# Kernel tuning notes

Hardware: AMD Instinct MI355X
Metric: run time of the kernel (lower is better)

The kernel has to match this reference:

```python
import jax, jax.numpy as jnp
import numpy as np

NUM_HEADS = 8


def setup_inputs() -> dict:
    key = jax.random.key(0)
    ks = jax.random.split(key, 5)
    b, c, h, w = 8, 256, 32, 32
    x = jax.random.normal(ks[0], (b, c, h, w), dtype=jnp.float32)
    w_qkv = jax.random.normal(ks[1], (3 * c, c), dtype=jnp.float32) * (c ** -0.5)
    b_qkv = jax.random.normal(ks[2], (3 * c,), dtype=jnp.float32) * 0.02
    w_proj = jax.random.normal(ks[3], (c, c), dtype=jnp.float32) * (c ** -0.5)
    b_proj = jax.random.normal(ks[4], (c,), dtype=jnp.float32) * 0.02
    return {"x": x, "w_qkv": w_qkv, "b_qkv": b_qkv, "w_proj": w_proj, "b_proj": b_proj}


def reference(x, w_qkv, b_qkv, w_proj, b_proj):
    b, c, h, w = x.shape
    nh = NUM_HEADS
    dh = c // nh
    L = h * w
    scale = dh ** -0.5
    # 1x1 conv == per-pixel GEMM
    qkv = jnp.einsum('bchw,oc->bohw', x, w_qkv) + b_qkv[None, :, None, None]
    qkv = qkv.reshape(b, 3, nh, dh, L)
    q, k, v = qkv[:, 0], qkv[:, 1], qkv[:, 2]  # each (b, nh, dh, L)
    attn = jnp.einsum('bhdi,bhdj->bhij', q, k) * scale  # (b, nh, L, L)
    attn = jax.nn.softmax(attn, axis=-1)
    out = jnp.einsum('bhdj,bhij->bhdi', v, attn)  # (b, nh, dh, L)
    out = out.reshape(b, c, h, w)
    proj = jnp.einsum('bchw,oc->bohw', out, w_proj) + b_proj[None, :, None, None]
    return x + proj
```

## Files before the change

kernel.cpp:

```cpp
#include <hip/hip_runtime.h>
#include <math.h>

#define B_   8
#define CIN  256
#define L_   1024
#define NH_  8
#define DH_  32

typedef __attribute__((ext_vector_type(8))) short short8;
typedef __attribute__((ext_vector_type(4))) short short4v;
typedef __attribute__((ext_vector_type(4))) float f32x4;
typedef __attribute__((ext_vector_type(16))) float f32x16;
typedef __attribute__((ext_vector_type(4))) unsigned int uint4v;

__device__ inline short f2bf_hu(float f) {
    union { float f; unsigned u; } v; v.f = f;
    return (short)((v.u + 0x8000u) >> 16);
}
__device__ inline float bf2f(short s) {
    union { unsigned u; float f; } v; v.u = ((unsigned)(unsigned short)s) << 16;
    return v.f;
}
__device__ inline unsigned pkbf2(float a, float b) {
    union { float f; unsigned u; } x, y; x.f = a; y.f = b;
    return __builtin_amdgcn_perm(y.u + 0x8000u, x.u + 0x8000u, 0x07060302u);
}

__global__ __launch_bounds__(256) void qkv_gemm(
    const float* __restrict__ x, const float* __restrict__ wq,
    const float* __restrict__ bias, short* __restrict__ qkv3)
{
    __shared__ __align__(16) short Xs[2][64][40];
    __shared__ __align__(16) short Wt[2][128][32];
    const int t = threadIdx.x, lane = t & 63, wv = t >> 6;
    const int n = lane & 15, quad = lane >> 4;
    const int b = blockIdx.z, o0 = blockIdx.y * 128, l0 = blockIdx.x * 64;

    float bias_r[8];
    #pragma unroll
    for (int nf = 0; nf < 8; nf++) bias_r[nf] = bias[o0 + nf * 16 + n];

    f32x4 acc[8];
    #pragma unroll
    for (int nf = 0; nf < 8; nf++) acc[nf] = (f32x4){0.f, 0.f, 0.f, 0.f};

    const int cS = t >> 3, lsS = (t & 7) * 8;

    const int ow = t >> 1, hw = t & 1;
    const float* wp = wq + (size_t)(o0 + ow) * 256 + hw * 16;
    const int wssw = (ow >> 1) & 3;
    float4 wr0, wr1, wr2, wr3;
    auto loadW = [&]() {
        wr0 = ((const float4*)wp)[0]; wr1 = ((const float4*)wp)[1];
        wr2 = ((const float4*)wp)[2]; wr3 = ((const float4*)wp)[3];
        wp += 32;
    };
    auto wwrite = [&](int buf) {
        uint4v pa = { pkbf2(wr0.x, wr0.y), pkbf2(wr0.z, wr0.w),
                      pkbf2(wr1.x, wr1.y), pkbf2(wr1.z, wr1.w) };
        uint4v pb = { pkbf2(wr2.x, wr2.y), pkbf2(wr2.z, wr2.w),
                      pkbf2(wr3.x, wr3.y), pkbf2(wr3.z, wr3.w) };
        *(uint4v*)&Wt[buf][ow][((hw * 2)     ^ wssw) * 8] = pa;
        *(uint4v*)&Wt[buf][ow][((hw * 2 + 1) ^ wssw) * 8] = pb;
    };

    auto xwrite = [&](int buf, const float4& a, const float4& c) {
        const float vals[8] = {a.x, a.y, a.z, a.w, c.x, c.y, c.z, c.w};
        #pragma unroll
        for (int k = 0; k < 8; k++) {
            const int ll = lsS + k;
            const int col = (((cS >> 3) ^ (ll & 3)) << 3) | (cS & 7);
            Xs[buf][ll][col] = f2bf_hu(vals[k]);
        }
    };

    const float* xp = &x[(((size_t)b * CIN + cS) << 10) + l0 + lsS];
    float4 xa = *(const float4*)xp, xb = *(const float4*)(xp + 4);
    loadW();
    xwrite(0, xa, xb);
    wwrite(0);
    xp += (size_t)32 << 10;
    xa = *(const float4*)xp; xb = *(const float4*)(xp + 4);
    loadW();

    const int wsw = (quad ^ ((n >> 1) & 3)) * 8;
    const int arow = wv * 16 + n;
    const int xsw = (quad ^ (arow & 3)) * 8;

    #pragma unroll
    for (int it = 0; it < 8; it++) {
        const int cur = it & 1;
        __syncthreads();
        const short8 af = *(const short8*)&Xs[cur][arow][xsw];
        #pragma unroll
        for (int nf = 0; nf < 8; nf++) {
            const short8 bf = *(const short8*)&Wt[cur][nf * 16 + n][wsw];
            acc[nf] = __builtin_amdgcn_mfma_f32_16x16x32_bf16(af, bf, acc[nf], 0, 0, 0);
        }
        if (it < 7) {
            xwrite(cur ^ 1, xa, xb);
            wwrite(cur ^ 1);
            if (it < 6) {
                xp += (size_t)32 << 10;
                xa = *(const float4*)xp; xb = *(const float4*)(xp + 4);
                loadW();
            }
        }
    }

    #pragma unroll
    for (int reg = 0; reg < 4; reg++) {
        const size_t l = l0 + wv * 16 + quad * 4 + reg;
        #pragma unroll
        for (int nf = 0; nf < 8; nf++) {
            const int o = o0 + nf * 16;
            const int tpl = o >> 8, hh = (o >> 5) & 7, dh0 = o & 31;
            short* dst = qkv3 + (((size_t)(tpl * 64 + b * 8 + hh)) << 15)
                              + l * 32 + dh0 + n;
            *dst = f2bf_hu(acc[nf][reg] + bias_r[nf]);
        }
    }
}

__global__ __launch_bounds__(256) void proj_gemm(
    const short* __restrict__ partO, const float* __restrict__ partD,
    const float* __restrict__ wq, const float* __restrict__ bias,
    const float* __restrict__ resid, float* __restrict__ out)
{
    __shared__ __align__(16) short Xs[2][64][40];
    __shared__ __align__(16) short Wt[2][64][32];
    const int t = threadIdx.x, lane = t & 63, wv = t >> 6;
    const int n = lane & 15, quad = lane >> 4;
    const int b = blockIdx.z, o0 = blockIdx.y * 64, l0 = blockIdx.x * 64;

    float bias_r[4];
    #pragma unroll
    for (int reg = 0; reg < 4; reg++) bias_r[reg] = bias[o0 + wv * 16 + quad * 4 + reg];

    f32x4 acc[4];
    #pragma unroll
    for (int nf = 0; nf < 4; nf++) acc[nf] = (f32x4){0.f, 0.f, 0.f, 0.f};

    const int l = t >> 2, cs = (t & 3) * 8;
    const size_t li = ((size_t)b << 10) + l0 + l;
    const short* p0 = &partO[(0 * (size_t)B_ * L_ + li) * CIN + cs];
    const short* p1 = &partO[(1 * (size_t)B_ * L_ + li) * CIN + cs];
    const float* pd0 = &partD[(0 * (size_t)B_ * L_ + li) * NH_];
    const float* pd1 = &partD[(1 * (size_t)B_ * L_ + li) * NH_];

    const int ow = t >> 2, cw = t & 3;
    const float* wp = wq + (size_t)(o0 + ow) * 256 + cw * 8;
    const int wpos = (cw ^ ((ow >> 1) & 3)) * 8;
    float4 wa, wb;
    auto loadW = [&]() {
        wa = ((const float4*)wp)[0]; wb = ((const float4*)wp)[1];
        wp += 32;
    };
    auto wwrite = [&](int buf) {
        uint4v pw = { pkbf2(wa.x, wa.y), pkbf2(wa.z, wa.w),
                      pkbf2(wb.x, wb.y), pkbf2(wb.z, wb.w) };
        *(uint4v*)&Wt[buf][ow][wpos] = pw;
    };

    short8 s0, s1;
    float d0, d1;
    auto combine_write = [&](int buf) {
        const float inv = 1.f / (d0 + d1);
        float v[8];
        #pragma unroll
        for (int e = 0; e < 8; e++) v[e] = (bf2f(s0[e]) + bf2f(s1[e])) * inv;
        uint4v pw = { pkbf2(v[0], v[1]), pkbf2(v[2], v[3]),
                      pkbf2(v[4], v[5]), pkbf2(v[6], v[7]) };
        *(uint4v*)&Xs[buf][l][cs] = pw;
    };

    s0 = *(const short8*)p0; s1 = *(const short8*)p1;
    d0 = pd0[0]; d1 = pd1[0];
    loadW();
    combine_write(0);
    wwrite(0);
    p0 += 32; p1 += 32;
    s0 = *(const short8*)p0; s1 = *(const short8*)p1;
    d0 = pd0[1]; d1 = pd1[1];
    loadW();

    const int wsw = (quad ^ ((n >> 1) & 3)) * 8;
    #pragma unroll
    for (int it = 0; it < 8; it++) {
        const int cur = it & 1;
        __syncthreads();
        const short8 af = *(const short8*)&Wt[cur][wv * 16 + n][wsw];
        #pragma unroll
        for (int nf = 0; nf < 4; nf++) {
            const short8 bf = *(const short8*)&Xs[cur][nf * 16 + n][quad * 8];
            acc[nf] = __builtin_amdgcn_mfma_f32_16x16x32_bf16(af, bf, acc[nf], 0, 0, 0);
        }
        if (it < 7) {
            combine_write(cur ^ 1);
            wwrite(cur ^ 1);
            if (it < 6) {
                p0 += 32; p1 += 32;
                s0 = *(const short8*)p0; s1 = *(const short8*)p1;
                d0 = pd0[it + 2]; d1 = pd1[it + 2];
                loadW();
            }
        }
    }

    #pragma unroll
    for (int reg = 0; reg < 4; reg++) {
        const int o = o0 + wv * 16 + quad * 4 + reg;
        #pragma unroll
        for (int nf = 0; nf < 4; nf++) {
            const size_t off = (((size_t)b * CIN + o) << 10) + l0 + nf * 16 + n;
            out[off] = acc[nf][reg] + bias_r[reg] + resid[off];
        }
    }
}

__global__ __launch_bounds__(256) void attn_mfma(
    const short* __restrict__ qkv3, short* __restrict__ partO,
    float* __restrict__ partD)
{
    __shared__ short Vt[2][32][80];

    const int t = threadIdx.x, lane = t & 63, wv = t >> 6;
    const int il = lane & 31, h2 = lane >> 5;
    const int id = blockIdx.x;
    const int bh = id & 63;
    const int b = bh >> 3, h = bh & 7;
    const int i0 = ((id >> 6) & 7) * 128;
    const int s  = id >> 9;

    const short* qbase = qkv3 + ((size_t)(b * 8 + h) << 15);
    const short* kbase = qbase + ((size_t)64 << 15);
    const short* vbase = qbase + ((size_t)128 << 15);

    const short* qp = qbase + (size_t)(i0 + wv * 32 + il) * 32 + h2 * 8;
    const short8 qa0 = *(const short8*)qp;
    const short8 qa1 = *(const short8*)(qp + 16);

    f32x16 o_acc = {0.f,0.f,0.f,0.f,0.f,0.f,0.f,0.f,
                    0.f,0.f,0.f,0.f,0.f,0.f,0.f,0.f};
    float dsum = 0.f;

    const float K1 = 0.25503510f;
    const float K2 = 11.54156036f;
    const int TSTRIDE = 64 * 32;
    const size_t soff = (size_t)s * 8 * TSTRIDE;

    const short* kp = kbase + soff + (size_t)il * 32 + h2 * 8;

    const int jS = t >> 3, dsS = (t & 7) * 4;
    const short* vp0 = vbase + soff + (size_t)jS * 32 + dsS;
    const short* vp1 = vp0 + 32 * 32;

    const int vmsk = ((dsS >> 2) & 7) << 3;
    const int vwo0 = dsS * 80 + (jS ^ vmsk);
    const int vwo1 = dsS * 80 + ((jS + 32) ^ vmsk);
    short* const vtb0 = &Vt[0][0][0];
    short* const vtb1 = &Vt[1][0][0];

    const int rmsk = ((il >> 2) & 7) << 3;
    int vro2[2][4];
    #pragma unroll
    for (int js = 0; js < 2; js++)
        #pragma unroll
        for (int g = 0; g < 4; g++)
            vro2[js][g] = il * 80 + ((js * 32 + g * 8 + 4 * h2) ^ rmsk);

    short8 kfA[4], kfB[4];

    auto stageV = [&](short* vtb) {
        const short4v a = *(const short4v*)vp0; vp0 += TSTRIDE;
        const short4v c = *(const short4v*)vp1; vp1 += TSTRIDE;
        #pragma unroll
        for (int u = 0; u < 4; u++) {
            vtb[vwo0 + u * 80] = a[u];
            vtb[vwo1 + u * 80] = c[u];
        }
    };
    auto loadK = [&](short8* kf) {
        kf[0] = *(const short8*)kp;
        kf[1] = *(const short8*)(kp + 16);
        kf[2] = *(const short8*)(kp + 1024);
        kf[3] = *(const short8*)(kp + 1024 + 16);
        kp += TSTRIDE;
    };
    auto tile = [&](const short8* kf, const short* vtb) {
        #pragma unroll
        for (int js = 0; js < 2; js++) {
            const f32x16 Z = {0.f,0.f,0.f,0.f,0.f,0.f,0.f,0.f,
                              0.f,0.f,0.f,0.f,0.f,0.f,0.f,0.f};
            f32x16 sv = __builtin_amdgcn_mfma_f32_32x32x16_bf16(kf[js*2],   qa0, Z,  0, 0, 0);
            sv        = __builtin_amdgcn_mfma_f32_32x32x16_bf16(kf[js*2+1], qa1, sv, 0, 0, 0);
            unsigned c[8];
            #pragma unroll
            for (int pi = 0; pi < 8; pi++) {
                const float pl = __builtin_amdgcn_exp2f(fmaf(sv[2*pi],   K1, -K2));
                const float ph = __builtin_amdgcn_exp2f(fmaf(sv[2*pi+1], K1, -K2));
                dsum += pl; dsum += ph;
                c[pi] = pkbf2(pl, ph);
            }
            union { unsigned u[4]; short8 s8; } pa0, pa1;
            pa0.u[0] = c[0]; pa0.u[1] = c[1]; pa0.u[2] = c[2]; pa0.u[3] = c[3];
            pa1.u[0] = c[4]; pa1.u[1] = c[5]; pa1.u[2] = c[6]; pa1.u[3] = c[7];
            union { short4v h4[2]; short8 s8; } vf0, vf1;
            vf0.h4[0] = *(const short4v*)(vtb + vro2[js][0]);
            vf0.h4[1] = *(const short4v*)(vtb + vro2[js][1]);
            o_acc = __builtin_amdgcn_mfma_f32_32x32x16_bf16(pa0.s8, vf0.s8, o_acc, 0, 0, 0);
            vf1.h4[0] = *(const short4v*)(vtb + vro2[js][2]);
            vf1.h4[1] = *(const short4v*)(vtb + vro2[js][3]);
            o_acc = __builtin_amdgcn_mfma_f32_32x32x16_bf16(pa1.s8, vf1.s8, o_acc, 0, 0, 0);
        }
    };

    stageV(vtb0);
    loadK(kfA);

    for (int itp = 0; itp < 4; itp++) {
        __syncthreads();
        stageV(vtb1);
        loadK(kfB);
        tile(kfA, vtb0);
        __syncthreads();
        if (itp < 3) { stageV(vtb0); loadK(kfA); }
        tile(kfB, vtb1);
    }

    const float dtot = dsum + __shfl_xor(dsum, 32);
    #pragma unroll
    for (int r = 0; r < 16; r++) {
        const int irow = (r & 3) + 8 * (r >> 2) + 4 * h2;
        const int ig = i0 + wv * 32 + irow;
        partO[(((size_t)s * B_ + b) * L_ + ig) * CIN + h * DH_ + il]
            = f2bf_hu(o_acc[r]);
    }
    if (lane < 32)
        partD[(((size_t)s * B_ + b) * L_ + (i0 + wv * 32 + il)) * NH_ + h] = dtot;
}

extern "C" void kernel_launch(void* const* d_in, const int* in_sizes, int n_in,
                              void* d_out, int out_size, void* d_ws, size_t ws_size,
                              hipStream_t stream) {
    const float* x      = (const float*)d_in[0];
    const float* w_qkv  = (const float*)d_in[1];
    const float* b_qkv  = (const float*)d_in[2];
    const float* w_proj = (const float*)d_in[3];
    const float* b_proj = (const float*)d_in[4];
    float* out = (float*)d_out;

    short* qkv3  = (short*)d_ws;
    short* partO = qkv3 + (size_t)B_ * L_ * 768;
    float* partD = (float*)(partO + (size_t)2 * B_ * L_ * CIN);

    qkv_gemm<<<dim3(16, 6, B_), 256, 0, stream>>>(x, w_qkv, b_qkv, qkv3);
    attn_mfma<<<dim3(1024), 256, 0, stream>>>(qkv3, partO, partD);
    proj_gemm<<<dim3(16, 4, B_), 256, 0, stream>>>(partO, partD, w_proj,
                                                   b_proj, x, out);
}
```

Before: 106.0 us.

## Remove split-K attention partials and normalize in attention epilogue

Attention blocks now process the full key range instead of two halves. Each block normalizes its output by the softmax denominator and writes a single bf16 O tensor. The projection GEMM reads this tensor directly and no longer combines two partial outputs and denominators. This removes the extra partial buffers and the combine arithmetic, but halves the attention grid to 512 blocks, which reduces parallelism and latency hiding.

```diff
diff --git a/kernel.cpp b/kernel.cpp
--- a/kernel.cpp
+++ b/kernel.cpp
@@ -123,9 +123,9 @@
 }
 
 __global__ __launch_bounds__(256) void proj_gemm(
-    const short* __restrict__ partO, const float* __restrict__ partD,
-    const float* __restrict__ wq, const float* __restrict__ bias,
-    const float* __restrict__ resid, float* __restrict__ out)
+    const short* __restrict__ O, const float* __restrict__ wq,
+    const float* __restrict__ bias, const float* __restrict__ resid,
+    float* __restrict__ out)
 {
     __shared__ __align__(16) short Xs[2][64][40];
     __shared__ __align__(16) short Wt[2][64][32];
@@ -142,11 +142,7 @@
     for (int nf = 0; nf < 4; nf++) acc[nf] = (f32x4){0.f, 0.f, 0.f, 0.f};
 
     const int l = t >> 2, cs = (t & 3) * 8;
-    const size_t li = ((size_t)b << 10) + l0 + l;
-    const short* p0 = &partO[(0 * (size_t)B_ * L_ + li) * CIN + cs];
-    const short* p1 = &partO[(1 * (size_t)B_ * L_ + li) * CIN + cs];
-    const float* pd0 = &partD[(0 * (size_t)B_ * L_ + li) * NH_];
-    const float* pd1 = &partD[(1 * (size_t)B_ * L_ + li) * NH_];
+    const short* p0 = &O[(((size_t)b << 10) + l0 + l) * CIN + cs];
 
     const int ow = t >> 2, cw = t & 3;
     const float* wp = wq + (size_t)(o0 + ow) * 256 + cw * 8;
@@ -162,26 +158,15 @@
         *(uint4v*)&Wt[buf][ow][wpos] = pw;
     };
 
-    short8 s0, s1;
-    float d0, d1;
-    auto combine_write = [&](int buf) {
-        const float inv = 1.f / (d0 + d1);
-        float v[8];
-        #pragma unroll
-        for (int e = 0; e < 8; e++) v[e] = (bf2f(s0[e]) + bf2f(s1[e])) * inv;
-        uint4v pw = { pkbf2(v[0], v[1]), pkbf2(v[2], v[3]),
-                      pkbf2(v[4], v[5]), pkbf2(v[6], v[7]) };
-        *(uint4v*)&Xs[buf][l][cs] = pw;
-    };
-
-    s0 = *(const short8*)p0; s1 = *(const short8*)p1;
-    d0 = pd0[0]; d1 = pd1[0];
+    short8 s0;
+    auto xwrite = [&](int buf) { *(short8*)&Xs[buf][l][cs] = s0; };
+
+    s0 = *(const short8*)p0;
     loadW();
-    combine_write(0);
+    xwrite(0);
     wwrite(0);
-    p0 += 32; p1 += 32;
-    s0 = *(const short8*)p0; s1 = *(const short8*)p1;
-    d0 = pd0[1]; d1 = pd1[1];
+    p0 += 32;
+    s0 = *(const short8*)p0;
     loadW();
 
     const int wsw = (quad ^ ((n >> 1) & 3)) * 8;
@@ -196,12 +181,11 @@
             acc[nf] = __builtin_amdgcn_mfma_f32_16x16x32_bf16(af, bf, acc[nf], 0, 0, 0);
         }
         if (it < 7) {
-            combine_write(cur ^ 1);
+            xwrite(cur ^ 1);
             wwrite(cur ^ 1);
             if (it < 6) {
-                p0 += 32; p1 += 32;
-                s0 = *(const short8*)p0; s1 = *(const short8*)p1;
-                d0 = pd0[it + 2]; d1 = pd1[it + 2];
+                p0 += 32;
+                s0 = *(const short8*)p0;
                 loadW();
             }
         }
@@ -219,18 +203,17 @@
 }
 
 __global__ __launch_bounds__(256) void attn_mfma(
-    const short* __restrict__ qkv3, short* __restrict__ partO,
-    float* __restrict__ partD)
+    const short* __restrict__ qkv3, short* __restrict__ O)
 {
     __shared__ short Vt[2][32][80];
+    __shared__ float Ds[4][32];
 
     const int t = threadIdx.x, lane = t & 63, wv = t >> 6;
     const int il = lane & 31, h2 = lane >> 5;
     const int id = blockIdx.x;
     const int bh = id & 63;
     const int b = bh >> 3, h = bh & 7;
-    const int i0 = ((id >> 6) & 7) * 128;
-    const int s  = id >> 9;
+    const int i0 = (id >> 6) * 128;
 
     const short* qbase = qkv3 + ((size_t)(b * 8 + h) << 15);
     const short* kbase = qbase + ((size_t)64 << 15);
@@ -247,12 +230,11 @@
     const float K1 = 0.25503510f;
     const float K2 = 11.54156036f;
     const int TSTRIDE = 64 * 32;
-    const size_t soff = (size_t)s * 8 * TSTRIDE;
-
-    const short* kp = kbase + soff + (size_t)il * 32 + h2 * 8;
+
+    const short* kp = kbase + (size_t)il * 32 + h2 * 8;
 
     const int jS = t >> 3, dsS = (t & 7) * 4;
-    const short* vp0 = vbase + soff + (size_t)jS * 32 + dsS;
+    const short* vp0 = vbase + (size_t)jS * 32 + dsS;
     const short* vp1 = vp0 + 32 * 32;
 
     const int vmsk = ((dsS >> 2) & 7) << 3;
@@ -318,26 +300,25 @@
     stageV(vtb0);
     loadK(kfA);
 
-    for (int itp = 0; itp < 4; itp++) {
+    for (int itp = 0; itp < 8; itp++) {
         __syncthreads();
         stageV(vtb1);
         loadK(kfB);
         tile(kfA, vtb0);
         __syncthreads();
-        if (itp < 3) { stageV(vtb0); loadK(kfA); }
+        if (itp < 7) { stageV(vtb0); loadK(kfA); }
         tile(kfB, vtb1);
     }
 
     const float dtot = dsum + __shfl_xor(dsum, 32);
+    if (h2 == 0) Ds[wv][il] = 1.f / dtot;
     #pragma unroll
     for (int r = 0; r < 16; r++) {
         const int irow = (r & 3) + 8 * (r >> 2) + 4 * h2;
         const int ig = i0 + wv * 32 + irow;
-        partO[(((size_t)s * B_ + b) * L_ + ig) * CIN + h * DH_ + il]
-            = f2bf_hu(o_acc[r]);
-    }
-    if (lane < 32)
-        partD[(((size_t)s * B_ + b) * L_ + (i0 + wv * 32 + il)) * NH_ + h] = dtot;
+        O[(((size_t)b << 10) + ig) * CIN + h * DH_ + il]
+            = f2bf_hu(o_acc[r] * Ds[wv][irow]);
+    }
 }
 
 extern "C" void kernel_launch(void* const* d_in, const int* in_sizes, int n_in,
@@ -350,12 +331,10 @@
     const float* b_proj = (const float*)d_in[4];
     float* out = (float*)d_out;
 
-    short* qkv3  = (short*)d_ws;
-    short* partO = qkv3 + (size_t)B_ * L_ * 768;
-    float* partD = (float*)(partO + (size_t)2 * B_ * L_ * CIN);
+    short* qkv3 = (short*)d_ws;
+    short* Obuf = qkv3 + (size_t)B_ * L_ * 768;
 
     qkv_gemm<<<dim3(16, 6, B_), 256, 0, stream>>>(x, w_qkv, b_qkv, qkv3);
-    attn_mfma<<<dim3(1024), 256, 0, stream>>>(qkv3, partO, partD);
-    proj_gemm<<<dim3(16, 4, B_), 256, 0, stream>>>(partO, partD, w_proj,
-                                                   b_proj, x, out);
-}
+    attn_mfma<<<dim3(512), 256, 0, stream>>>(qkv3, Obuf);
+    proj_gemm<<<dim3(16, 4, B_), 256, 0, stream>>>(Obuf, w_proj, b_proj, x, out);
+}
```

New measurement: 109.3 us. +3.1%, slower.
